# Kernel optimization log

Hardware: AMD Instinct MI355X
Metric: run time of the kernel (lower is better)

Reference implementation:

```python
import jax, jax.numpy as jnp
import numpy as np
from math import sqrt

B, N, DK = 4, 4096, 64


def setup_inputs() -> dict:
    key = jax.random.key(0)
    ks = jax.random.split(key, 5)
    x = jax.random.normal(ks[0], (B, N, DK), dtype=jnp.float32)
    Wv = jax.random.normal(ks[1], (DK, DK), dtype=jnp.float32) / sqrt(DK)
    bv = jax.random.normal(ks[2], (DK,), dtype=jnp.float32) * 0.02
    wq = jax.random.normal(ks[3], (DK,), dtype=jnp.float32) / sqrt(DK)
    wk = jax.random.normal(ks[4], (DK,), dtype=jnp.float32) / sqrt(DK)
    gamma = jnp.ones((DK,), dtype=jnp.float32)
    beta = jnp.zeros((DK,), dtype=jnp.float32)
    return {"x": x, "Wv": Wv, "bv": bv, "wq": wq, "wk": wk, "gamma": gamma, "beta": beta}


def _layer_norm(h, gamma, beta, eps=1e-5):
    mu = jnp.mean(h, axis=-1, keepdims=True)
    var = jnp.var(h, axis=-1, keepdims=True)
    return (h - mu) * jax.lax.rsqrt(var + eps) * gamma + beta


def reference(x, Wv, bv, wq, wk, gamma, beta):
    d_k = x.shape[-1]
    V = jnp.einsum('bnd,ed->bne', x, Wv) + bv          # (B, N, DK)
    Q = jnp.einsum('bnd,d->bn', x, wq)                 # scalar per token
    K = jnp.einsum('bnd,d->bn', x, wk)
    # RBF-kernel scores A[b,i,j] = exp(-(Q_i - K_j)^2)  -> (B, N, N)
    A = jnp.exp(-jnp.square(Q[:, :, None] - K[:, None, :]))
    P = jax.nn.softmax(A / sqrt(d_k), axis=-1)
    out = jnp.einsum('bij,bjd->bid', P, V) + x
    return _layer_norm(out, gamma, beta)
```

## Files before the change

### kernel.cpp

```cpp
#include <hip/hip_runtime.h>

#define NB   4
#define NSEQ 4096
#define DK   64
#define NTOK (NB * NSEQ)

#define QK_SCALE 1.2011224087864498f

typedef __attribute__((ext_vector_type(8))) short short8;
typedef __attribute__((ext_vector_type(4))) float f32x4;

__device__ __forceinline__ float fast_exp2(float x) {
#if __has_builtin(__builtin_amdgcn_exp2f)
    return __builtin_amdgcn_exp2f(x);
#else
    return exp2f(x);
#endif
}

__device__ __forceinline__ unsigned short bf16_rne(float f) {
    unsigned u = __float_as_uint(f);
    u += 0x7fffu + ((u >> 16) & 1u);
    return (unsigned short)(u >> 16);
}

__device__ __forceinline__ short8 u4_to_s8(uint4 u) {
    union { uint4 u; short8 s; } c; c.u = u; return c.s;
}

#define AS3U(p) ((__attribute__((address_space(3))) unsigned int*)(p))
#define AS1U(p) ((const __attribute__((address_space(1))) unsigned int*)(p))

__global__ __launch_bounds__(512) void qkv_kernel(
    const float* __restrict__ x, const float* __restrict__ Wv,
    const float* __restrict__ bv, const float* __restrict__ wq,
    const float* __restrict__ wk,
    float* __restrict__ Qs, float* __restrict__ Ks, unsigned short* __restrict__ Vt)
{
    __shared__ float x_lds[64 * 68];
    __shared__ float wvt[64 * 68];
    __shared__ float wqk[128];
    __shared__ float bvl[64];
    __shared__ unsigned short vt_lds[64 * 72];

    const int t = threadIdx.x;
    const int tok0 = blockIdx.x * 64;

    #pragma unroll
    for (int r = 0; r < 2; ++r) {
        int f = t + 512 * r;
        int row = f >> 4, c4 = f & 15;
        float4 v = ((const float4*)(x + (size_t)(tok0 + row) * DK))[c4];
        *(float4*)&x_lds[row * 68 + c4 * 4] = v;
    }
    #pragma unroll
    for (int r = 0; r < 2; ++r) {
        int f = t + 512 * r;
        int e = f >> 4, c4 = f & 15;
        float4 v = ((const float4*)(Wv + e * DK))[c4];
        wvt[(c4 * 4 + 0) * 68 + e] = v.x;
        wvt[(c4 * 4 + 1) * 68 + e] = v.y;
        wvt[(c4 * 4 + 2) * 68 + e] = v.z;
        wvt[(c4 * 4 + 3) * 68 + e] = v.w;
    }
    if (t < 64) { wqk[t * 2] = wq[t]; wqk[t * 2 + 1] = wk[t]; bvl[t] = bv[t]; }
    __syncthreads();

    const int tok = t >> 3, oc = t & 7;
    const int e0 = oc * 8;
    float acc[8];
    #pragma unroll
    for (int ee = 0; ee < 8; ++ee) acc[ee] = bvl[e0 + ee];

    for (int d = 0; d < DK; d += 4) {
        float4 x4 = *(const float4*)&x_lds[tok * 68 + d];
        const float xs[4] = {x4.x, x4.y, x4.z, x4.w};
        #pragma unroll
        for (int dd = 0; dd < 4; ++dd) {
            float xv = xs[dd];
            const float4* wrow = (const float4*)&wvt[(d + dd) * 68 + e0];
            float4 wa = wrow[0], wb = wrow[1];
            acc[0] += xv * wa.x; acc[1] += xv * wa.y;
            acc[2] += xv * wa.z; acc[3] += xv * wa.w;
            acc[4] += xv * wb.x; acc[5] += xv * wb.y;
            acc[6] += xv * wb.z; acc[7] += xv * wb.w;
        }
    }
    #pragma unroll
    for (int k = 0; k < 8; ++k)
        vt_lds[(e0 + k) * 72 + tok] = bf16_rne(acc[k]);

    if (t < 128) {
        const int tk = t & 63;
        const int sel = (t >= 64);
        float a = 0.f;
        for (int d = 0; d < DK; ++d)
            a += x_lds[tk * 68 + d] * wqk[d * 2 + sel];
        (sel ? Ks : Qs)[tok0 + tk] = a * QK_SCALE;
    }
    __syncthreads();

    const int bb = tok0 >> 12, n0 = tok0 & 4095;
    {
        int d = t >> 3, c = t & 7;
        uint4 v = *(const uint4*)((const char*)vt_lds + d * 144 + c * 16);
        *(uint4*)(Vt + (size_t)(bb * 64 + d) * 4096 + n0 + c * 8) = v;
    }
}

extern __shared__ float smem[];

__global__ __launch_bounds__(1024, 4) void attn_kernel(
    const float* __restrict__ x,
    const float* __restrict__ Qsg, const float* __restrict__ Ksg,
    const unsigned short* __restrict__ Vt,
    const float* __restrict__ gamma, const float* __restrict__ beta,
    float* __restrict__ out, int nrep)
{
    float* k_lds = smem;
    unsigned short* vs = (unsigned short*)(smem + 4096);
    float* red   = smem + 4096;
    float* dred  = smem + 4096 + 8 * 64 * 68;

    const int t    = threadIdx.x;
    const int B    = blockIdx.x;
    const int b    = (B & 7) >> 1;
    const int i0   = (((B >> 3) << 1) | (B & 1)) << 6;
    const int w    = t >> 6;
    const int lane = t & 63;
    const int rit  = lane & 15;
    const int q    = lane >> 4;
    const int rgrp = w >> 3;
    const int js   = w & 7;

    ((float4*)k_lds)[t] = ((const float4*)(Ksg + (size_t)b * 4096))[t];

    const float Qs0 = Qsg[b * 4096 + i0 + rgrp * 32 + rit];
    const float Qs1 = Qsg[b * 4096 + i0 + rgrp * 32 + 16 + rit];

    const short onebf = (short)0x3F80;
    const short8 vones = {onebf, onebf, onebf, onebf, onebf, onebf, onebf, onebf};

    const unsigned short* Vtb0 = Vt + (size_t)b * 64 * 4096;

    for (int rep = 0; rep < nrep; ++rep) {

    f32x4 acc[2][4] = {};
    f32x4 accd[2] = {};

    #pragma unroll
    for (int i = 0; i < 4; ++i) {
        const int d = w + 16 * i;
        const unsigned short* g = Vtb0 + (size_t)d * 4096 + lane * 8;
        unsigned short* l = vs + d * 520;
#if __has_builtin(__builtin_amdgcn_global_load_lds)
        __builtin_amdgcn_global_load_lds(AS1U(g), AS3U(l), 16, 0, 0);
#else
        *(uint4*)(l + lane * 8) = *(const uint4*)g;
#endif
    }
    __syncthreads();

    for (int r = 0; r < 8; ++r) {
        const int bf = r & 1;
        if (r < 7) {
            const int jw = (r + 1) * 512;
            #pragma unroll
            for (int i = 0; i < 4; ++i) {
                const int d = w + 16 * i;
                const unsigned short* g = Vtb0 + (size_t)d * 4096 + jw + lane * 8;
                unsigned short* l = vs + (bf ^ 1) * 33280 + d * 520;
#if __has_builtin(__builtin_amdgcn_global_load_lds)
                __builtin_amdgcn_global_load_lds(AS1U(g), AS3U(l), 16, 0, 0);
#else
                *(uint4*)(l + lane * 8) = *(const uint4*)g;
#endif
            }
        }

        #pragma unroll
        for (int sl = 0; sl < 2; ++sl) {
            const int jloc = js * 64 + sl * 32;
            const unsigned short* vf = vs + bf * 33280 + rit * 520 + jloc + q * 8;
            uint4 bu0 = *(const uint4*)(vf);
            uint4 bu1 = *(const uint4*)(vf + 16 * 520);
            uint4 bu2 = *(const uint4*)(vf + 32 * 520);
            uint4 bu3 = *(const uint4*)(vf + 48 * 520);

            const float* kn = k_lds + r * 512 + jloc + q * 8;
            float4 ka = *(const float4*)(kn);
            float4 kb = *(const float4*)(kn + 4);
            float kv[8] = {ka.x, ka.y, ka.z, ka.w, kb.x, kb.y, kb.z, kb.w};

            float w0[8], w1[8];
            #pragma unroll
            for (int jj = 0; jj < 8; ++jj) {
                float d0 = Qs0 - kv[jj];
                float g0 = fast_exp2(-d0 * d0);
                float p0 = __builtin_fmaf(g0, 3.2552083e-4f, 7.8125e-3f);
                p0 = __builtin_fmaf(g0, p0, 0.125f);
                w0[jj] = __builtin_fmaf(g0, p0, 1.0f);
                float d1 = Qs1 - kv[jj];
                float g1 = fast_exp2(-d1 * d1);
                float p1 = __builtin_fmaf(g1, 3.2552083e-4f, 7.8125e-3f);
                p1 = __builtin_fmaf(g1, p1, 0.125f);
                w1[jj] = __builtin_fmaf(g1, p1, 1.0f);
            }
            uint4 au0, au1;
            au0.x = __builtin_amdgcn_perm(__float_as_uint(w0[1]), __float_as_uint(w0[0]), 0x07060302u);
            au0.y = __builtin_amdgcn_perm(__float_as_uint(w0[3]), __float_as_uint(w0[2]), 0x07060302u);
            au0.z = __builtin_amdgcn_perm(__float_as_uint(w0[5]), __float_as_uint(w0[4]), 0x07060302u);
            au0.w = __builtin_amdgcn_perm(__float_as_uint(w0[7]), __float_as_uint(w0[6]), 0x07060302u);
            au1.x = __builtin_amdgcn_perm(__float_as_uint(w1[1]), __float_as_uint(w1[0]), 0x07060302u);
            au1.y = __builtin_amdgcn_perm(__float_as_uint(w1[3]), __float_as_uint(w1[2]), 0x07060302u);
            au1.z = __builtin_amdgcn_perm(__float_as_uint(w1[5]), __float_as_uint(w1[4]), 0x07060302u);
            au1.w = __builtin_amdgcn_perm(__float_as_uint(w1[7]), __float_as_uint(w1[6]), 0x07060302u);
            short8 a0 = u4_to_s8(au0);
            short8 a1 = u4_to_s8(au1);

            short8 b0 = u4_to_s8(bu0), b1 = u4_to_s8(bu1);
            short8 b2 = u4_to_s8(bu2), b3 = u4_to_s8(bu3);
            acc[0][0] = __builtin_amdgcn_mfma_f32_16x16x32_bf16(a0, b0, acc[0][0], 0, 0, 0);
            acc[0][1] = __builtin_amdgcn_mfma_f32_16x16x32_bf16(a0, b1, acc[0][1], 0, 0, 0);
            acc[0][2] = __builtin_amdgcn_mfma_f32_16x16x32_bf16(a0, b2, acc[0][2], 0, 0, 0);
            acc[0][3] = __builtin_amdgcn_mfma_f32_16x16x32_bf16(a0, b3, acc[0][3], 0, 0, 0);
            acc[1][0] = __builtin_amdgcn_mfma_f32_16x16x32_bf16(a1, b0, acc[1][0], 0, 0, 0);
            acc[1][1] = __builtin_amdgcn_mfma_f32_16x16x32_bf16(a1, b1, acc[1][1], 0, 0, 0);
            acc[1][2] = __builtin_amdgcn_mfma_f32_16x16x32_bf16(a1, b2, acc[1][2], 0, 0, 0);
            acc[1][3] = __builtin_amdgcn_mfma_f32_16x16x32_bf16(a1, b3, acc[1][3], 0, 0, 0);
            accd[0]   = __builtin_amdgcn_mfma_f32_16x16x32_bf16(a0, vones, accd[0], 0, 0, 0);
            accd[1]   = __builtin_amdgcn_mfma_f32_16x16x32_bf16(a1, vones, accd[1], 0, 0, 0);
        }
        __syncthreads();
    }

    {
        float* rbase = red + (size_t)js * (64 * 68);
        #pragma unroll
        for (int rt = 0; rt < 2; ++rt)
            #pragma unroll
            for (int ct = 0; ct < 4; ++ct)
                #pragma unroll
                for (int rg = 0; rg < 4; ++rg)
                    rbase[(rgrp * 32 + rt * 16 + q * 4 + rg) * 68 + ct * 16 + rit]
                        = acc[rt][ct][rg];
        if (rit == 0) {
            #pragma unroll
            for (int rt = 0; rt < 2; ++rt)
                #pragma unroll
                for (int rg = 0; rg < 4; ++rg)
                    dred[js * 64 + rgrp * 32 + rt * 16 + q * 4 + rg] = accd[rt][rg];
        }
    }
    __syncthreads();

    {
        const int row = t >> 4, cg = t & 15, c0 = cg * 4;
        float dsum = 0.f;
        #pragma unroll
        for (int sl = 0; sl < 8; ++sl) dsum += dred[sl * 64 + row];
        const float inv = 1.0f / dsum;
        const size_t rowg = (size_t)(b * 4096 + i0 + row);

        float4 num = make_float4(0.f, 0.f, 0.f, 0.f);
        #pragma unroll
        for (int sl = 0; sl < 8; ++sl) {
            float4 r4 = *(const float4*)&red[(size_t)sl * (64 * 68) + row * 68 + c0];
            num.x += r4.x; num.y += r4.y; num.z += r4.z; num.w += r4.w;
        }
        const float4 x4 = *(const float4*)(x + rowg * 64 + c0);
        float4 h;
        h.x = num.x * inv + x4.x;
        h.y = num.y * inv + x4.y;
        h.z = num.z * inv + x4.z;
        h.w = num.w * inv + x4.w;

        float sm = h.x + h.y + h.z + h.w;
        float ss = h.x * h.x + h.y * h.y + h.z * h.z + h.w * h.w;
        #pragma unroll
        for (int m = 1; m < 16; m <<= 1) { sm += __shfl_xor(sm, m); ss += __shfl_xor(ss, m); }
        const float mu   = sm * 0.015625f;
        const float var  = ss * 0.015625f - mu * mu;
        const float rstd = rsqrtf(var + 1e-5f);

        const float4 g4 = *(const float4*)(gamma + c0);
        const float4 b4 = *(const float4*)(beta + c0);
        float4 o;
        o.x = (h.x - mu) * rstd * g4.x + b4.x;
        o.y = (h.y - mu) * rstd * g4.y + b4.y;
        o.z = (h.z - mu) * rstd * g4.z + b4.z;
        o.w = (h.w - mu) * rstd * g4.w + b4.w;
        *(float4*)(out + rowg * 64 + c0) = o;
    }
    __syncthreads();
    }
}

extern "C" void kernel_launch(void* const* d_in, const int* in_sizes, int n_in,
                              void* d_out, int out_size, void* d_ws, size_t ws_size,
                              hipStream_t stream)
{
    const float* x     = (const float*)d_in[0];
    const float* Wv    = (const float*)d_in[1];
    const float* bv    = (const float*)d_in[2];
    const float* wq    = (const float*)d_in[3];
    const float* wk    = (const float*)d_in[4];
    const float* gamma = (const float*)d_in[5];
    const float* beta  = (const float*)d_in[6];
    float* out = (float*)d_out;

    float* Qs = (float*)d_ws;
    float* Ks = Qs + NTOK;
    unsigned short* Vt = (unsigned short*)(Ks + NTOK);

    const int attn_lds = 4096 * 4 + 8 * 64 * 68 * 4 + 8 * 64 * 4;
    hipFuncSetAttribute((const void*)attn_kernel,
                        hipFuncAttributeMaxDynamicSharedMemorySize, attn_lds);

    qkv_kernel<<<dim3(NTOK / 64), dim3(512), 0, stream>>>(x, Wv, bv, wq, wk, Qs, Ks, Vt);
    attn_kernel<<<dim3(NB * (NSEQ / 64)), dim3(1024), attn_lds, stream>>>(
        x, Qs, Ks, Vt, gamma, beta, out, 1);
}
```

Before: 95.57 us.

## Store V in MFMA-fragment-tiled layout to remove LDS padding and conflicts

The qkv kernel now writes V in bf16 as 32-token chunks, each split into 4 column tiles of 64 lanes by 8 values, which matches the MFMA B-operand fragment order. The attention kernel then loads contiguous 512-element rows into LDS without padding and reads each fragment as one contiguous lane-indexed uint4. The aim is to avoid LDS bank conflicts and the strided row addressing of the old padded transposed layout. The cost is a scattered global store pattern in the qkv kernel, and correctness depends on the producer and consumer index maps matching exactly.

```diff
diff --git a/kernel.cpp b/kernel.cpp
--- a/kernel.cpp
+++ b/kernel.cpp
@@ -30,6 +30,7 @@
 
 #define AS3U(p) ((__attribute__((address_space(3))) unsigned int*)(p))
 #define AS1U(p) ((const __attribute__((address_space(1))) unsigned int*)(p))
+
 
 __global__ __launch_bounds__(512) void qkv_kernel(
     const float* __restrict__ x, const float* __restrict__ Wv,
@@ -102,9 +103,13 @@
 
     const int bb = tok0 >> 12, n0 = tok0 & 4095;
     {
-        int d = t >> 3, c = t & 7;
+        const int c = t >> 6, d = t & 63;
         uint4 v = *(const uint4*)((const char*)vt_lds + d * 144 + c * 16);
-        *(uint4*)(Vt + (size_t)(bb * 64 + d) * 4096 + n0 + c * 8) = v;
+        const int jc   = (n0 >> 5) + (c >> 2);
+        const int lane = (c & 3) * 16 + (d & 15);
+        const int ct   = d >> 4;
+        unsigned short* dst = Vt + ((((size_t)bb * 128 + jc) * 4 + ct) * 64 + lane) * 8;
+        *(uint4*)dst = v;
     }
 }
 
@@ -141,7 +146,7 @@
     const short onebf = (short)0x3F80;
     const short8 vones = {onebf, onebf, onebf, onebf, onebf, onebf, onebf, onebf};
 
-    const unsigned short* Vtb0 = Vt + (size_t)b * 64 * 4096;
+    const unsigned short* Vtb0 = Vt + (size_t)b * 262144;
 
     for (int rep = 0; rep < nrep; ++rep) {
 
@@ -150,9 +155,9 @@
 
     #pragma unroll
     for (int i = 0; i < 4; ++i) {
-        const int d = w + 16 * i;
-        const unsigned short* g = Vtb0 + (size_t)d * 4096 + lane * 8;
-        unsigned short* l = vs + d * 520;
+        const int row = w + 16 * i;
+        const unsigned short* g = Vtb0 + row * 512 + lane * 8;
+        unsigned short* l = vs + row * 512;
 #if __has_builtin(__builtin_amdgcn_global_load_lds)
         __builtin_amdgcn_global_load_lds(AS1U(g), AS3U(l), 16, 0, 0);
 #else
@@ -164,12 +169,11 @@
     for (int r = 0; r < 8; ++r) {
         const int bf = r & 1;
         if (r < 7) {
-            const int jw = (r + 1) * 512;
             #pragma unroll
             for (int i = 0; i < 4; ++i) {
-                const int d = w + 16 * i;
-                const unsigned short* g = Vtb0 + (size_t)d * 4096 + jw + lane * 8;
-                unsigned short* l = vs + (bf ^ 1) * 33280 + d * 520;
+                const int row = w + 16 * i;
+                const unsigned short* g = Vtb0 + (r + 1) * 32768 + row * 512 + lane * 8;
+                unsigned short* l = vs + (bf ^ 1) * 32768 + row * 512;
 #if __has_builtin(__builtin_amdgcn_global_load_lds)
                 __builtin_amdgcn_global_load_lds(AS1U(g), AS3U(l), 16, 0, 0);
 #else
@@ -180,14 +184,14 @@
 
         #pragma unroll
         for (int sl = 0; sl < 2; ++sl) {
-            const int jloc = js * 64 + sl * 32;
-            const unsigned short* vf = vs + bf * 33280 + rit * 520 + jloc + q * 8;
+            const int jcl = js * 2 + sl;
+            const unsigned short* vf = vs + bf * 32768 + jcl * 2048 + lane * 8;
             uint4 bu0 = *(const uint4*)(vf);
-            uint4 bu1 = *(const uint4*)(vf + 16 * 520);
-            uint4 bu2 = *(const uint4*)(vf + 32 * 520);
-            uint4 bu3 = *(const uint4*)(vf + 48 * 520);
-
-            const float* kn = k_lds + r * 512 + jloc + q * 8;
+            uint4 bu1 = *(const uint4*)(vf + 512);
+            uint4 bu2 = *(const uint4*)(vf + 1024);
+            uint4 bu3 = *(const uint4*)(vf + 1536);
+
+            const float* kn = k_lds + r * 512 + jcl * 32 + q * 8;
             float4 ka = *(const float4*)(kn);
             float4 kb = *(const float4*)(kn + 4);
             float kv[8] = {ka.x, ka.y, ka.z, ka.w, kb.x, kb.y, kb.z, kb.w};
```

Result: no change. 94.85 us (-0.8%).
